# Kernel optimization log

Measured on AMD Instinct MI355X. Metric: run time of the kernel, lower is better.

The kernel has to match this reference:

```python
import jax, jax.numpy as jnp
import numpy as np

# dims (match init_kwargs / input_specs)
IN = 128      # input_size / num_features
GH = 512      # global_hidden_size
GL = 3        # global_nlayers
NH = 128      # effective noise hidden (DFRNN kwarg noise_nlayers, due to arg swap)
NL = 2        # effective noise layers (DFRNN kwarg noise_hidden_size, due to arg swap)
NF = 10       # n_global_factors
NT = 1024     # num_ts
T = 192       # num_periods


def _cell(x, W, bi, bh):
    # single LSTM step from zero state: c0=h0=0 => f-gate and W_hh drop out
    g = x @ W.T + bi + bh                      # [n, 4H]
    i, f, c, o = jnp.split(g, 4, axis=-1)      # torch gate order i,f,g,o
    cc = jax.nn.sigmoid(i) * jnp.tanh(c)
    return jax.nn.sigmoid(o) * jnp.tanh(cc)


def _stack(x, Wih0, bih0, bhh0, Wih, bih, bhh):
    h = _cell(x, Wih0, bih0, bhh0)
    for l in range(Wih.shape[0]):              # small fixed layer count
        h = _cell(h, Wih[l], bih[l], bhh[l])
    return h


def setup_inputs() -> dict:
    key = jax.random.key(0)
    ks = jax.random.split(key, 16)
    s = 0.05
    return {
        "X": jax.random.normal(ks[0], (NT, T, IN), jnp.float32),
        # global-factor LSTM params
        "g_Wih0": s * jax.random.normal(ks[1], (4 * GH, IN), jnp.float32),
        "g_bih0": s * jax.random.normal(ks[2], (4 * GH,), jnp.float32),
        "g_bhh0": s * jax.random.normal(ks[3], (4 * GH,), jnp.float32),
        "g_Wih": s * jax.random.normal(ks[4], (GL - 1, 4 * GH, GH), jnp.float32),
        "g_bih": s * jax.random.normal(ks[5], (GL - 1, 4 * GH), jnp.float32),
        "g_bhh": s * jax.random.normal(ks[6], (GL - 1, 4 * GH), jnp.float32),
        # embed linear (global_hidden_size -> n_global_factors)
        "e_W": s * jax.random.normal(ks[7], (NF, GH), jnp.float32),
        "e_b": s * jax.random.normal(ks[8], (NF,), jnp.float32),
        # noise LSTM params
        "n_Wih0": s * jax.random.normal(ks[9], (4 * NH, IN), jnp.float32),
        "n_bih0": s * jax.random.normal(ks[10], (4 * NH,), jnp.float32),
        "n_bhh0": s * jax.random.normal(ks[11], (4 * NH,), jnp.float32),
        "n_Wih": s * jax.random.normal(ks[12], (NL - 1, 4 * NH, NH), jnp.float32),
        "n_bih": s * jax.random.normal(ks[13], (NL - 1, 4 * NH), jnp.float32),
        "n_bhh": s * jax.random.normal(ks[14], (NL - 1, 4 * NH), jnp.float32),
        # noise affine head (NH -> 1)
        "a_W": s * jax.random.normal(ks[15], (1, NH), jnp.float32),
        "a_b": jnp.zeros((1,), jnp.float32),
    }


def reference(X, g_Wih0, g_bih0, g_bhh0, g_Wih, g_bih, g_bhh, e_W, e_b,
              n_Wih0, n_bih0, n_bhh0, n_Wih, n_bih, n_bhh, a_W, a_b):
    nt, t, f = X.shape
    Z = X.reshape(nt * t, f)                                   # all (ts, period) tokens, loop vectorized
    # DeepFactor branch: gt = relu(last-layer h), factor linear is dead code
    gt = jax.nn.relu(_stack(Z, g_Wih0, g_bih0, g_bhh0, g_Wih, g_bih, g_bhh))
    mu = (gt @ e_W.T + e_b).sum(axis=-1).reshape(nt, t)        # embed then sum over factors
    # Noise branch
    hn = jax.nn.relu(_stack(Z, n_Wih0, n_bih0, n_bhh0, n_Wih, n_bih, n_bhh))
    st = hn @ a_W.T + a_b                                      # [nt*t, 1]
    sigma = jnp.log1p(jnp.exp(st)).reshape(nt, t) + 1e-6       # log(1+exp) + eps
    return mu, sigma
```

## Files before the change

### kernel.cpp

```cpp
#include <hip/hip_runtime.h>

#define IN_F  128
#define GHID  512
#define NHID  128
#define NTOK  196608L
#define LDSP  520

#define L2E 1.4426950408889634f

typedef __attribute__((ext_vector_type(8))) short short8;
typedef __attribute__((ext_vector_type(4))) float floatx4;

#define O_GW0 0L
#define O_GW1 196608L
#define O_GW2 983040L
#define O_NW0 1769472L
#define O_NW1 1818624L
#define NWS   1867776L
#define F_GB0 0
#define F_GB1 1536
#define F_GB2 3072
#define F_NB0 4608
#define F_NB1 4992
#define F_WE  5376
#define F_AW  5888
#define F_BE  6016
#define F_AB  6017

__device__ __forceinline__ unsigned short f2bf(float f) {
  unsigned int u = __float_as_uint(f);
  u += 0x7fffu + ((u >> 16) & 1u);
  return (unsigned short)(u >> 16);
}

__device__ __forceinline__ long srcoff(long pp, int H, int K) {
  long f = pp >> 9;
  int r = (int)(pp & 511);
  int ln = r >> 3, j = r & 7;
  int nKT = K >> 5, nCT = H >> 4;
  int tk = (int)(f % nKT);
  long t2 = f / nKT;
  int tn = (int)(t2 % nCT);
  int gate = (int)(t2 / nCT);
  int n = tn * 16 + (ln & 15);
  int k = tk * 32 + ((ln >> 4) << 3) + j;
  int go = (gate == 0) ? 0 : ((gate == 1) ? 2 * H : 3 * H);
  return (long)(go + n) * K + k;
}

__global__ void prep_kernel(
    const float* __restrict__ gW0, const float* __restrict__ gbi0, const float* __restrict__ gbh0,
    const float* __restrict__ gW,  const float* __restrict__ gbi,  const float* __restrict__ gbh,
    const float* __restrict__ eW,  const float* __restrict__ eb,
    const float* __restrict__ nW0, const float* __restrict__ nbi0, const float* __restrict__ nbh0,
    const float* __restrict__ nW,  const float* __restrict__ nbi,  const float* __restrict__ nbh,
    const float* __restrict__ aW,  const float* __restrict__ ab,
    unsigned short* __restrict__ wpk, float* __restrict__ fpk)
{
  long idx = (long)blockIdx.x * blockDim.x + threadIdx.x;
  if (idx < NWS) {
    const float* src;
    long off;
    if (idx < O_GW1)      { off = srcoff(idx - O_GW0, 512, 128); src = gW0; }
    else if (idx < O_GW2) { off = srcoff(idx - O_GW1, 512, 512); src = gW; }
    else if (idx < O_NW0) { off = srcoff(idx - O_GW2, 512, 512); src = gW + 1048576; }
    else if (idx < O_NW1) { off = srcoff(idx - O_NW0, 128, 128); src = nW0; }
    else                  { off = srcoff(idx - O_NW1, 128, 128); src = nW; }
    wpk[idx] = f2bf(src[off]);
    return;
  }
  long p = idx - NWS;
  if (p < 1536) { int g = (int)(p >> 9), n = (int)(p & 511);
    int o = (g == 0 ? 0 : (g == 1 ? 1024 : 1536)) + n;
    fpk[F_GB0 + p] = gbi0[o] + gbh0[o]; return; }
  p -= 1536;
  if (p < 1536) { int g = (int)(p >> 9), n = (int)(p & 511);
    int o = (g == 0 ? 0 : (g == 1 ? 1024 : 1536)) + n;
    fpk[F_GB1 + p] = gbi[o] + gbh[o]; return; }
  p -= 1536;
  if (p < 1536) { int g = (int)(p >> 9), n = (int)(p & 511);
    int o = (g == 0 ? 0 : (g == 1 ? 1024 : 1536)) + n;
    fpk[F_GB2 + p] = gbi[2048 + o] + gbh[2048 + o]; return; }
  p -= 1536;
  if (p < 384) { int g = (int)(p / 128), n = (int)(p % 128);
    int o = (g == 0 ? 0 : (g == 1 ? 256 : 384)) + n;
    fpk[F_NB0 + p] = nbi0[o] + nbh0[o]; return; }
  p -= 384;
  if (p < 384) { int g = (int)(p / 128), n = (int)(p % 128);
    int o = (g == 0 ? 0 : (g == 1 ? 256 : 384)) + n;
    fpk[F_NB1 + p] = nbi[o] + nbh[o]; return; }
  p -= 384;
  if (p < 512) { float s = 0.f;
    for (int f = 0; f < 10; ++f) s += eW[f * 512 + p];
    fpk[F_WE + p] = s; return; }
  p -= 512;
  if (p < 128) { fpk[F_AW + p] = aW[p]; return; }
  p -= 128;
  if (p == 0) { float s = 0.f; for (int f = 0; f < 10; ++f) s += eb[f]; fpk[F_BE] = s; return; }
  if (p == 1) { fpk[F_AB] = ab[0]; return; }
}

__device__ __forceinline__ float cell_h(float gi, float gc, float go) {
  float ei = __builtin_amdgcn_exp2f(gi * -L2E);
  float u  = __builtin_amdgcn_exp2f(gc * (2.0f * L2E));
  float eo = __builtin_amdgcn_exp2f(go * -L2E);
  float r1 = __builtin_amdgcn_rcpf((u + 1.f) * (1.f + ei));
  float cc = (u - 1.f) * r1;
  float s  = cc * cc;
  float num = cc * fmaf(10.f, s, 105.f);
  float den = fmaf(s, s + 45.f, 105.f);
  return num * __builtin_amdgcn_rcpf(den * (1.f + eo));
}

template <int K, int H, int TT, int CPW, int NW, int MODE>
__device__ __forceinline__ void layer_run(
    const unsigned short* __restrict__ sIn,
    unsigned short* __restrict__ sOut,
    const unsigned short* __restrict__ wp,
    const float* __restrict__ bias,
    const float* __restrict__ dotw,
    float* accVec,
    int colTile0, int tokBase, int lane)
{
  constexpr int nKT = K / 32;
  constexpr int nCT = H / 16;
#pragma unroll
  for (int cp = 0; cp < CPW; ++cp) {
    int tn = colTile0 + cp * NW;
    int colg = tn * 16 + (lane & 15);
    const unsigned short* p0 = wp + (size_t)tn * nKT * 512 + lane * 8;
    const unsigned short* p1 = p0 + (size_t)nCT * nKT * 512;
    const unsigned short* p2 = p1 + (size_t)nCT * nKT * 512;
    short8 b0 = *(const short8*)(p0);
    short8 b1 = *(const short8*)(p1);
    short8 b2 = *(const short8*)(p2);
    float bi = bias[colg], bc = bias[H + colg], bo = bias[2 * H + colg];
    floatx4 acc[3][TT];
#pragma unroll
    for (int tt = 0; tt < TT; ++tt) {
      acc[0][tt] = (floatx4){bi, bi, bi, bi};
      acc[1][tt] = (floatx4){bc, bc, bc, bc};
      acc[2][tt] = (floatx4){bo, bo, bo, bo};
    }
    const unsigned short* aRow = sIn + (size_t)(tokBase + (lane & 15)) * LDSP + ((lane >> 4) << 3);
#pragma unroll 1
    for (int ks = 0; ks < nKT; ++ks) {
      int nks = (ks + 1 < nKT) ? (ks + 1) : ks;
      short8 nb0 = *(const short8*)(p0 + (size_t)nks * 512);
      short8 nb1 = *(const short8*)(p1 + (size_t)nks * 512);
      short8 nb2 = *(const short8*)(p2 + (size_t)nks * 512);
      short8 a[TT];
#pragma unroll
      for (int tt = 0; tt < TT; ++tt)
        a[tt] = *(const short8*)(aRow + (size_t)tt * 16 * LDSP + ks * 32);
#pragma unroll
      for (int tt = 0; tt < TT; ++tt) {
        acc[0][tt] = __builtin_amdgcn_mfma_f32_16x16x32_bf16(a[tt], b0, acc[0][tt], 0, 0, 0);
        acc[1][tt] = __builtin_amdgcn_mfma_f32_16x16x32_bf16(a[tt], b1, acc[1][tt], 0, 0, 0);
        acc[2][tt] = __builtin_amdgcn_mfma_f32_16x16x32_bf16(a[tt], b2, acc[2][tt], 0, 0, 0);
      }
      b0 = nb0; b1 = nb1; b2 = nb2;
    }
    float dw = 0.f;
    if constexpr (MODE == 1) dw = dotw[colg];
    int rbase = tokBase + ((lane >> 4) << 2);
#pragma unroll
    for (int tt = 0; tt < TT; ++tt) {
      float vr[4];
#pragma unroll
      for (int r = 0; r < 4; ++r) {
        float h = cell_h(acc[0][tt][r], acc[1][tt][r], acc[2][tt][r]);
        if constexpr (MODE == 0) {
          sOut[(size_t)(rbase + tt * 16 + r) * LDSP + colg] = f2bf(h);
        } else {
          vr[r] = fmaxf(h, 0.f) * dw;
        }
      }
      if constexpr (MODE == 1) {
#pragma unroll
        for (int r = 0; r < 4; ++r) {
          float v = vr[r];
          v += __shfl_xor(v, 1, 16);
          v += __shfl_xor(v, 2, 16);
          v += __shfl_xor(v, 4, 16);
          v += __shfl_xor(v, 8, 16);
          if ((lane & 15) == 0)
            atomicAdd(&accVec[tokBase + tt * 16 + ((lane >> 4) << 2) + r], v);
        }
      }
    }
  }
}

__attribute__((amdgpu_waves_per_eu(4, 4)))
__global__ __launch_bounds__(1024) void dfrnn_main(
    const float* __restrict__ X,
    const unsigned short* __restrict__ wpk,
    const float* __restrict__ fpk,
    float* __restrict__ out)
{
  __shared__ __align__(16) unsigned short bufA[64 * LDSP];
  __shared__ __align__(16) unsigned short bufB[64 * LDSP];
  __shared__ float accMu[64];
  __shared__ float accSt[64];
  int tid = threadIdx.x;
  int wave = tid >> 6, lane = tid & 63;
  size_t blkTok = (size_t)blockIdx.x * 64;

  if (tid < 64) { accMu[tid] = 0.f; accSt[tid] = 0.f; }
  for (int i = tid; i < 64 * 32; i += 1024) {
    int row = i >> 5, c4 = i & 31;
    float4 v = *(const float4*)(X + (blkTok + row) * 128 + c4 * 4);
    ushort4 b;
    b.x = f2bf(v.x); b.y = f2bf(v.y); b.z = f2bf(v.z); b.w = f2bf(v.w);
    *(ushort4*)&bufA[(size_t)row * LDSP + c4 * 4] = b;
  }
  __syncthreads();

  layer_run<128, 128, 2, 1, 8, 0>(bufA, bufA + 128, wpk + O_NW0, fpk + F_NB0,
                                  nullptr, nullptr, wave & 7, (wave >> 3) * 32, lane);
  __syncthreads();

  layer_run<128, 128, 2, 1, 8, 1>(bufA + 128, nullptr, wpk + O_NW1, fpk + F_NB1,
                                  fpk + F_AW, accSt, wave & 7, (wave >> 3) * 32, lane);
  layer_run<128, 512, 4, 2, 16, 0>(bufA, bufB, wpk + O_GW0, fpk + F_GB0,
                                   nullptr, nullptr, wave, 0, lane);
  __syncthreads();

  layer_run<512, 512, 4, 2, 16, 0>(bufB, bufA, wpk + O_GW1, fpk + F_GB1,
                                   nullptr, nullptr, wave, 0, lane);
  __syncthreads();

  layer_run<512, 512, 4, 2, 16, 1>(bufA, nullptr, wpk + O_GW2, fpk + F_GB2,
                                   fpk + F_WE, accMu, wave, 0, lane);
  __syncthreads();

  if (tid < 64) {
    float mu = accMu[tid] + fpk[F_BE];
    float st = accSt[tid] + fpk[F_AB];
    out[blkTok + tid] = mu;
    out[NTOK + blkTok + tid] = log1pf(__expf(st)) + 1e-6f;
  }
}

extern "C" void kernel_launch(void* const* d_in, const int* in_sizes, int n_in,
                              void* d_out, int out_size, void* d_ws, size_t ws_size,
                              hipStream_t stream) {
  const float* X     = (const float*)d_in[0];
  const float* gW0   = (const float*)d_in[1];
  const float* gbi0  = (const float*)d_in[2];
  const float* gbh0  = (const float*)d_in[3];
  const float* gW    = (const float*)d_in[4];
  const float* gbi   = (const float*)d_in[5];
  const float* gbh   = (const float*)d_in[6];
  const float* eW    = (const float*)d_in[7];
  const float* eb    = (const float*)d_in[8];
  const float* nW0   = (const float*)d_in[9];
  const float* nbi0  = (const float*)d_in[10];
  const float* nbh0  = (const float*)d_in[11];
  const float* nW    = (const float*)d_in[12];
  const float* nbi   = (const float*)d_in[13];
  const float* nbh   = (const float*)d_in[14];
  const float* aW    = (const float*)d_in[15];
  const float* ab    = (const float*)d_in[16];

  unsigned short* wpk = (unsigned short*)d_ws;
  float* fpk = (float*)((char*)d_ws + NWS * 2);

  long prepTotal = NWS + 1536 * 3 + 384 * 2 + 512 + 128 + 2;
  int prepBlocks = (int)((prepTotal + 255) / 256);
  prep_kernel<<<prepBlocks, 256, 0, stream>>>(gW0, gbi0, gbh0, gW, gbi, gbh, eW, eb,
                                              nW0, nbi0, nbh0, nW, nbi, nbh, aW, ab,
                                              wpk, fpk);
  dfrnn_main<<<3072, 1024, 0, stream>>>(X, wpk, fpk, (float*)d_out);
}
```

Measured before the change: 980.8 us.

## Switch to 32x32x16 MFMA tiles with 512-thread blocks and repacked weights

Replaces the 16x16x32 bf16 MFMA with 32x32x16 tiles, repacks the weight layout to match, and halves the block to 8 waves with 2 waves per EU, so each wave covers more columns. Bigger MFMA tiles reuse each LDS A-fragment and weight fragment across more outputs, which cuts LDS and global weight traffic per FLOP. X is now read with nontemporal loads. The cost is more accumulator registers per wave (16 floats per tile), fewer waves to hide latency, and shuffle reductions plus atomics run per register across 32 lanes.

```diff
diff --git a/kernel.cpp b/kernel.cpp
--- a/kernel.cpp
+++ b/kernel.cpp
@@ -8,8 +8,9 @@
 
 #define L2E 1.4426950408889634f
 
-typedef __attribute__((ext_vector_type(8))) short short8;
-typedef __attribute__((ext_vector_type(4))) float floatx4;
+typedef __attribute__((ext_vector_type(8)))  short short8;
+typedef __attribute__((ext_vector_type(16))) float floatx16;
+typedef __attribute__((ext_vector_type(4)))  float f4;
 
 #define O_GW0 0L
 #define O_GW1 196608L
@@ -37,13 +38,13 @@
   long f = pp >> 9;
   int r = (int)(pp & 511);
   int ln = r >> 3, j = r & 7;
-  int nKT = K >> 5, nCT = H >> 4;
+  int nKT = K >> 4, nCT = H >> 5;
   int tk = (int)(f % nKT);
   long t2 = f / nKT;
   int tn = (int)(t2 % nCT);
   int gate = (int)(t2 / nCT);
-  int n = tn * 16 + (ln & 15);
-  int k = tk * 32 + ((ln >> 4) << 3) + j;
+  int n = tn * 32 + (ln & 31);
+  int k = tk * 16 + ((ln >> 5) << 3) + j;
   int go = (gate == 0) ? 0 : ((gate == 1) ? 2 * H : 3 * H);
   return (long)(go + n) * K + k;
 }
@@ -112,7 +113,7 @@
   return num * __builtin_amdgcn_rcpf(den * (1.f + eo));
 }
 
-template <int K, int H, int TT, int CPW, int NW, int MODE>
+template <int K, int H, int RT, int CPW, int NW, int MODE>
 __device__ __forceinline__ void layer_run(
     const unsigned short* __restrict__ sIn,
     unsigned short* __restrict__ sOut,
@@ -120,14 +121,14 @@
     const float* __restrict__ bias,
     const float* __restrict__ dotw,
     float* accVec,
-    int colTile0, int tokBase, int lane)
+    int colTile0, int rtBase, int lane)
 {
-  constexpr int nKT = K / 32;
-  constexpr int nCT = H / 16;
+  constexpr int nKT = K / 16;
+  constexpr int nCT = H / 32;
 #pragma unroll
   for (int cp = 0; cp < CPW; ++cp) {
     int tn = colTile0 + cp * NW;
-    int colg = tn * 16 + (lane & 15);
+    int colg = tn * 32 + (lane & 31);
     const unsigned short* p0 = wp + (size_t)tn * nKT * 512 + lane * 8;
     const unsigned short* p1 = p0 + (size_t)nCT * nKT * 512;
     const unsigned short* p2 = p1 + (size_t)nCT * nKT * 512;
@@ -135,65 +136,59 @@
     short8 b1 = *(const short8*)(p1);
     short8 b2 = *(const short8*)(p2);
     float bi = bias[colg], bc = bias[H + colg], bo = bias[2 * H + colg];
-    floatx4 acc[3][TT];
-#pragma unroll
-    for (int tt = 0; tt < TT; ++tt) {
-      acc[0][tt] = (floatx4){bi, bi, bi, bi};
-      acc[1][tt] = (floatx4){bc, bc, bc, bc};
-      acc[2][tt] = (floatx4){bo, bo, bo, bo};
+    floatx16 acc[3][RT];
+#pragma unroll
+    for (int rt = 0; rt < RT; ++rt) {
+#pragma unroll
+      for (int e = 0; e < 16; ++e) {
+        acc[0][rt][e] = bi; acc[1][rt][e] = bc; acc[2][rt][e] = bo;
+      }
     }
-    const unsigned short* aRow = sIn + (size_t)(tokBase + (lane & 15)) * LDSP + ((lane >> 4) << 3);
+    const unsigned short* aBase = sIn + (size_t)(rtBase + (lane & 31)) * LDSP + ((lane >> 5) << 3);
 #pragma unroll 1
     for (int ks = 0; ks < nKT; ++ks) {
       int nks = (ks + 1 < nKT) ? (ks + 1) : ks;
       short8 nb0 = *(const short8*)(p0 + (size_t)nks * 512);
       short8 nb1 = *(const short8*)(p1 + (size_t)nks * 512);
       short8 nb2 = *(const short8*)(p2 + (size_t)nks * 512);
-      short8 a[TT];
-#pragma unroll
-      for (int tt = 0; tt < TT; ++tt)
-        a[tt] = *(const short8*)(aRow + (size_t)tt * 16 * LDSP + ks * 32);
-#pragma unroll
-      for (int tt = 0; tt < TT; ++tt) {
-        acc[0][tt] = __builtin_amdgcn_mfma_f32_16x16x32_bf16(a[tt], b0, acc[0][tt], 0, 0, 0);
-        acc[1][tt] = __builtin_amdgcn_mfma_f32_16x16x32_bf16(a[tt], b1, acc[1][tt], 0, 0, 0);
-        acc[2][tt] = __builtin_amdgcn_mfma_f32_16x16x32_bf16(a[tt], b2, acc[2][tt], 0, 0, 0);
+      short8 a[RT];
+#pragma unroll
+      for (int rt = 0; rt < RT; ++rt)
+        a[rt] = *(const short8*)(aBase + (size_t)rt * 32 * LDSP + ks * 16);
+#pragma unroll
+      for (int rt = 0; rt < RT; ++rt) {
+        acc[0][rt] = __builtin_amdgcn_mfma_f32_32x32x16_bf16(a[rt], b0, acc[0][rt], 0, 0, 0);
+        acc[1][rt] = __builtin_amdgcn_mfma_f32_32x32x16_bf16(a[rt], b1, acc[1][rt], 0, 0, 0);
+        acc[2][rt] = __builtin_amdgcn_mfma_f32_32x32x16_bf16(a[rt], b2, acc[2][rt], 0, 0, 0);
       }
       b0 = nb0; b1 = nb1; b2 = nb2;
     }
     float dw = 0.f;
     if constexpr (MODE == 1) dw = dotw[colg];
-    int rbase = tokBase + ((lane >> 4) << 2);
-#pragma unroll
-    for (int tt = 0; tt < TT; ++tt) {
-      float vr[4];
-#pragma unroll
-      for (int r = 0; r < 4; ++r) {
-        float h = cell_h(acc[0][tt][r], acc[1][tt][r], acc[2][tt][r]);
+#pragma unroll
+    for (int rt = 0; rt < RT; ++rt) {
+#pragma unroll
+      for (int reg = 0; reg < 16; ++reg) {
+        int row = rtBase + rt * 32 + (reg & 3) + 8 * (reg >> 2) + 4 * (lane >> 5);
+        float h = cell_h(acc[0][rt][reg], acc[1][rt][reg], acc[2][rt][reg]);
         if constexpr (MODE == 0) {
-          sOut[(size_t)(rbase + tt * 16 + r) * LDSP + colg] = f2bf(h);
+          sOut[(size_t)row * LDSP + colg] = f2bf(h);
         } else {
-          vr[r] = fmaxf(h, 0.f) * dw;
-        }
-      }
-      if constexpr (MODE == 1) {
-#pragma unroll
-        for (int r = 0; r < 4; ++r) {
-          float v = vr[r];
-          v += __shfl_xor(v, 1, 16);
-          v += __shfl_xor(v, 2, 16);
-          v += __shfl_xor(v, 4, 16);
-          v += __shfl_xor(v, 8, 16);
-          if ((lane & 15) == 0)
-            atomicAdd(&accVec[tokBase + tt * 16 + ((lane >> 4) << 2) + r], v);
+          float v = fmaxf(h, 0.f) * dw;
+          v += __shfl_xor(v, 1, 32);
+          v += __shfl_xor(v, 2, 32);
+          v += __shfl_xor(v, 4, 32);
+          v += __shfl_xor(v, 8, 32);
+          v += __shfl_xor(v, 16, 32);
+          if ((lane & 31) == 0) atomicAdd(&accVec[row], v);
         }
       }
     }
   }
 }
 
-__attribute__((amdgpu_waves_per_eu(4, 4)))
-__global__ __launch_bounds__(1024) void dfrnn_main(
+__attribute__((amdgpu_waves_per_eu(2, 2)))
+__global__ __launch_bounds__(512) void dfrnn_main(
     const float* __restrict__ X,
     const unsigned short* __restrict__ wpk,
     const float* __restrict__ fpk,
@@ -208,31 +203,31 @@
   size_t blkTok = (size_t)blockIdx.x * 64;
 
   if (tid < 64) { accMu[tid] = 0.f; accSt[tid] = 0.f; }
-  for (int i = tid; i < 64 * 32; i += 1024) {
+  for (int i = tid; i < 64 * 32; i += 512) {
     int row = i >> 5, c4 = i & 31;
-    float4 v = *(const float4*)(X + (blkTok + row) * 128 + c4 * 4);
+    f4 v = __builtin_nontemporal_load((const f4*)(X + (blkTok + row) * 128 + c4 * 4));
     ushort4 b;
     b.x = f2bf(v.x); b.y = f2bf(v.y); b.z = f2bf(v.z); b.w = f2bf(v.w);
     *(ushort4*)&bufA[(size_t)row * LDSP + c4 * 4] = b;
   }
   __syncthreads();
 
-  layer_run<128, 128, 2, 1, 8, 0>(bufA, bufA + 128, wpk + O_NW0, fpk + F_NB0,
-                                  nullptr, nullptr, wave & 7, (wave >> 3) * 32, lane);
-  __syncthreads();
-
-  layer_run<128, 128, 2, 1, 8, 1>(bufA + 128, nullptr, wpk + O_NW1, fpk + F_NB1,
-                                  fpk + F_AW, accSt, wave & 7, (wave >> 3) * 32, lane);
-  layer_run<128, 512, 4, 2, 16, 0>(bufA, bufB, wpk + O_GW0, fpk + F_GB0,
-                                   nullptr, nullptr, wave, 0, lane);
-  __syncthreads();
-
-  layer_run<512, 512, 4, 2, 16, 0>(bufB, bufA, wpk + O_GW1, fpk + F_GB1,
-                                   nullptr, nullptr, wave, 0, lane);
-  __syncthreads();
-
-  layer_run<512, 512, 4, 2, 16, 1>(bufA, nullptr, wpk + O_GW2, fpk + F_GB2,
-                                   fpk + F_WE, accMu, wave, 0, lane);
+  layer_run<128, 128, 1, 1, 0, 0>(bufA, bufA + 128, wpk + O_NW0, fpk + F_NB0,
+                                  nullptr, nullptr, wave >> 1, (wave & 1) * 32, lane);
+  __syncthreads();
+
+  layer_run<128, 128, 1, 1, 0, 1>(bufA + 128, nullptr, wpk + O_NW1, fpk + F_NB1,
+                                  fpk + F_AW, accSt, wave >> 1, (wave & 1) * 32, lane);
+  layer_run<128, 512, 2, 2, 8, 0>(bufA, bufB, wpk + O_GW0, fpk + F_GB0,
+                                  nullptr, nullptr, wave, 0, lane);
+  __syncthreads();
+
+  layer_run<512, 512, 2, 2, 8, 0>(bufB, bufA, wpk + O_GW1, fpk + F_GB1,
+                                  nullptr, nullptr, wave, 0, lane);
+  __syncthreads();
+
+  layer_run<512, 512, 2, 2, 8, 1>(bufA, nullptr, wpk + O_GW2, fpk + F_GB2,
+                                  fpk + F_WE, accMu, wave, 0, lane);
   __syncthreads();
 
   if (tid < 64) {
@@ -272,5 +267,5 @@
   prep_kernel<<<prepBlocks, 256, 0, stream>>>(gW0, gbi0, gbh0, gW, gbi, gbh, eW, eb,
                                               nW0, nbi0, nbh0, nW, nbi, nbh, aW, ab,
                                               wpk, fpk);
-  dfrnn_main<<<3072, 1024, 0, stream>>>(X, wpk, fpk, (float*)d_out);
-}
+  dfrnn_main<<<3072, 512, 0, stream>>>(X, wpk, fpk, (float*)d_out);
+}
```

After: 1.221 ms. 1.24x slower.
